# Performance work log

Hardware: AMD Instinct MI355X
Metric: run time of the kernel (lower is better)

## Reference

```python
import jax, jax.numpy as jnp
import numpy as np

IN_DIM = 1024
OUT_DIM = 1024
NUM_COEFFS = 32 + 3  # grid_size + spline_order


def setup_inputs() -> dict:
    key = jax.random.key(0)
    k1, k2, k3 = jax.random.split(key, 3)
    x = jax.random.normal(k1, (4096, IN_DIM), dtype=jnp.float32)
    spline_weight = jax.random.normal(k2, (IN_DIM, OUT_DIM, NUM_COEFFS), dtype=jnp.float32) * 0.1
    base_scale = jax.random.normal(k3, (IN_DIM, OUT_DIM), dtype=jnp.float32) * 0.1
    grid = jnp.linspace(-1.0, 1.0, NUM_COEFFS, dtype=jnp.float32)
    return {"x": x, "spline_weight": spline_weight, "base_scale": base_scale, "grid": grid}


def _b_spline_cubic(x, grid):
    # x: [b, i] -> basis [b, i, c]
    h = 2.0 / (NUM_COEFFS - 1)
    dist = jnp.abs(x[..., None] - grid) / h
    inner = 2.0 / 3.0 - dist * dist + dist * dist * dist * 0.5
    t = 2.0 - dist
    outer = t * t * t / 6.0
    return jnp.where(dist < 1.0, inner, jnp.where(dist < 2.0, outer, 0.0))


def reference(x, spline_weight, base_scale, grid):
    x_norm = jnp.clip(x, -0.99, 0.99)
    base_act = jax.nn.silu(x_norm)                      # [b, i]
    base_out = jnp.einsum('bi,ij->bj', base_act, base_scale)
    basis = _b_spline_cubic(x_norm, grid)               # [b, i, c]
    spline_out = jnp.einsum('bic,ijc->bj', basis, spline_weight)
    return base_out + spline_out
```

## Files before the change

### kernel.cpp

```cpp
#include <hip/hip_runtime.h>
#include <hip/hip_bf16.h>


#define IN_DIM 1024
#define OUT_DIM 1024
#define NC 35
#define KPI 36
#define KTOT (IN_DIM * KPI)
#define MROWS 4096
#define BM 128
#define BN 128
#define BK 32
#define BKP 40
#define NSPLIT 4
#define KCH (KTOT / NSPLIT)
#define NSTEP (KCH / BK)

typedef __attribute__((ext_vector_type(8))) __bf16 bf16x8;
typedef __attribute__((ext_vector_type(4))) float f32x4;

__device__ __forceinline__ unsigned short f2bf(float f) {
  unsigned int u = __builtin_bit_cast(unsigned int, f);
  u = (u + 0x7FFFu + ((u >> 16) & 1u)) >> 16;
  return (unsigned short)u;
}

__global__ __launch_bounds__(256) void prep_wb(const float* __restrict__ sw,
                                               const float* __restrict__ bs,
                                               unsigned short* __restrict__ wb) {
  int id = blockIdx.x * 256 + threadIdx.x;
  int i = id & (IN_DIM - 1);
  int n = id >> 10;
  const float* s = sw + (size_t)i * (OUT_DIM * NC) + (size_t)n * NC;
  unsigned short v[KPI];
#pragma unroll
  for (int c = 0; c < NC; ++c) v[c] = f2bf(s[c]);
  v[NC] = f2bf(bs[(size_t)i * OUT_DIM + n]);
  uint2* dst = (uint2*)(wb + (size_t)n * KTOT + (size_t)i * KPI);
#pragma unroll
  for (int w = 0; w < 9; ++w) {
    uint2 t;
    t.x = (unsigned)v[4 * w + 0] | ((unsigned)v[4 * w + 1] << 16);
    t.y = (unsigned)v[4 * w + 2] | ((unsigned)v[4 * w + 3] << 16);
    dst[w] = t;
  }
}

template <bool USE_WB>
__global__ __launch_bounds__(256) void kan_gemm(const float* __restrict__ x,
                                                const unsigned short* __restrict__ wb,
                                                const float* __restrict__ sw,
                                                const float* __restrict__ bs,
                                                float* __restrict__ out) {
  __shared__ __align__(16) unsigned short As[BM * BKP];
  __shared__ __align__(16) unsigned short Ws[BN * BKP];

  const int tid = threadIdx.x;
  const int mt = blockIdx.x, nt = blockIdx.y, kc = blockIdx.z;

  const int sb = tid & 127;
  const int shalf = tid >> 7;
  const int klo = shalf * 16;
  const int wrow = tid >> 1;
  const int whal = tid & 1;
  const int lane = tid & 63;
  const int wid = tid >> 6;
  const int wm = (wid & 1) * 64;
  const int wn = (wid >> 1) * 64;
  const int lm = lane & 15;
  const int quad = lane >> 4;
  const int ko = quad * 8;

  f32x4 acc[4][4];
#pragma unroll
  for (int a = 0; a < 4; ++a)
#pragma unroll
    for (int b = 0; b < 4; ++b) acc[a][b] = f32x4{0.f, 0.f, 0.f, 0.f};

  const float* xrow = x + (size_t)(mt * BM + sb) * IN_DIM;

  for (int step = 0; step < NSTEP; ++step) {
    const int kbase = kc * KCH + step * BK;

    {
      uint4 z = make_uint4(0, 0, 0, 0);
      uint4* az = (uint4*)(&As[sb * BKP + klo]);
      az[0] = z;
      az[1] = z;
    }

    {
      const int ilo = kbase / KPI;
      const int ihi = (kbase + BK - 1) / KPI;
      for (int ii = ilo; ii <= ihi; ++ii) {
        float xv = xrow[ii];
        float xn = fminf(fmaxf(xv, -0.99f), 0.99f);
        float u = (xn + 1.0f) * 17.0f;
        float sf = floorf(u);
        int s = (int)sf;
        float f = u - sf, g = 1.0f - f;
        float f2 = f * f, g2 = g * g;
        float v0 = g2 * g * (1.f / 6.f);
        float v1 = 0.66666667f - f2 + 0.5f * f2 * f;
        float v2 = 0.66666667f - g2 + 0.5f * g2 * g;
        float v3 = f2 * f * (1.f / 6.f);
        float sig = xn / (1.0f + __expf(-xn));
        const int kb0 = ii * KPI - kbase;
#pragma unroll
        for (int t = 0; t < 4; ++t) {
          int c = s - 1 + t;
          float v = (t == 0) ? v0 : (t == 1) ? v1 : (t == 2) ? v2 : v3;
          int kq = kb0 + c;
          if (c >= 0 && c < NC && kq >= klo && kq < klo + 16)
            As[sb * BKP + kq] = f2bf(v);
        }
        int kqb = kb0 + NC;
        if (kqb >= klo && kqb < klo + 16) As[sb * BKP + kqb] = f2bf(sig);
      }
    }

    if (USE_WB) {
      const unsigned short* src = wb + (size_t)(nt * BN + wrow) * KTOT + kbase + whal * 16;
      uint4 w0 = ((const uint4*)src)[0];
      uint4 w1 = ((const uint4*)src)[1];
      uint4* wd = (uint4*)(&Ws[wrow * BKP + whal * 16]);
      wd[0] = w0;
      wd[1] = w1;
    } else {
      const int j = nt * BN + wrow;
      unsigned int p[8];
#pragma unroll
      for (int q = 0; q < 8; ++q) {
        unsigned int lohi = 0;
#pragma unroll
        for (int h = 0; h < 2; ++h) {
          int k = kbase + whal * 16 + q * 2 + h;
          int i = k / KPI;
          int c = k - i * KPI;
          float v = (c < NC) ? sw[(size_t)i * (OUT_DIM * NC) + (size_t)j * NC + c]
                             : bs[(size_t)i * OUT_DIM + j];
          lohi |= ((unsigned int)f2bf(v)) << (16 * h);
        }
        p[q] = lohi;
      }
      uint4* wd = (uint4*)(&Ws[wrow * BKP + whal * 16]);
      wd[0] = make_uint4(p[0], p[1], p[2], p[3]);
      wd[1] = make_uint4(p[4], p[5], p[6], p[7]);
    }

    __syncthreads();

    uint4 af[4], bfr[4];
#pragma unroll
    for (int mi = 0; mi < 4; ++mi)
      af[mi] = *(const uint4*)(&As[(wm + mi * 16 + lm) * BKP + ko]);
#pragma unroll
    for (int ni = 0; ni < 4; ++ni)
      bfr[ni] = *(const uint4*)(&Ws[(wn + ni * 16 + lm) * BKP + ko]);
#pragma unroll
    for (int mi = 0; mi < 4; ++mi)
#pragma unroll
      for (int ni = 0; ni < 4; ++ni)
        acc[mi][ni] = __builtin_amdgcn_mfma_f32_16x16x32_bf16(
            __builtin_bit_cast(bf16x8, af[mi]), __builtin_bit_cast(bf16x8, bfr[ni]),
            acc[mi][ni], 0, 0, 0);

    __syncthreads();
  }

#pragma unroll
  for (int mi = 0; mi < 4; ++mi)
#pragma unroll
    for (int ni = 0; ni < 4; ++ni)
#pragma unroll
      for (int r = 0; r < 4; ++r) {
        int row = mt * BM + wm + mi * 16 + quad * 4 + r;
        int col = nt * BN + wn + ni * 16 + lm;
        atomicAdd(&out[(size_t)row * OUT_DIM + col], acc[mi][ni][r]);
      }
}

extern "C" void kernel_launch(void* const* d_in, const int* in_sizes, int n_in,
                              void* d_out, int out_size, void* d_ws, size_t ws_size,
                              hipStream_t stream) {
  const float* x = (const float*)d_in[0];
  const float* sw = (const float*)d_in[1];
  const float* bs = (const float*)d_in[2];
  float* out = (float*)d_out;

  hipMemsetAsync(d_out, 0, (size_t)MROWS * OUT_DIM * sizeof(float), stream);

  const size_t WB_BYTES = (size_t)OUT_DIM * KTOT * sizeof(unsigned short);
  dim3 grid(MROWS / BM, OUT_DIM / BN, NSPLIT);
  if (ws_size >= WB_BYTES) {
    unsigned short* wbp = (unsigned short*)d_ws;
    prep_wb<<<(IN_DIM * OUT_DIM) / 256, 256, 0, stream>>>(sw, bs, wbp);
    kan_gemm<true><<<grid, 256, 0, stream>>>(x, wbp, sw, bs, out);
  } else {
    kan_gemm<false><<<grid, 256, 0, stream>>>(x, nullptr, sw, bs, out);
  }
}
```

Measured before the change: 855.9 us.

## Materialize spline basis in workspace and pipeline GEMM with direct-to-LDS loads

Adds a prep kernel that expands x into the bf16 B-spline basis plus SiLU term. It writes the result to the workspace in a K-chunk-major layout, with weights repacked the same way. A new 256x256-tile GEMM with 512 threads then streams both operands through a triple-buffered LDS ring using global_load_lds, so loads overlap the MFMA work. This removes the redundant per-tile basis computation and the register round trips. In exchange it adds an extra ~300MB of workspace traffic and uses unpadded LDS rows, which may cause bank conflicts. It only takes effect if the workspace is large enough.

```diff
diff --git a/kernel.cpp b/kernel.cpp
--- a/kernel.cpp
+++ b/kernel.cpp
@@ -7,14 +7,13 @@
 #define NC 35
 #define KPI 36
 #define KTOT (IN_DIM * KPI)
+#define NW (KTOT / 32)
 #define MROWS 4096
-#define BM 128
-#define BN 128
+#define BM 256
+#define BN 256
 #define BK 32
-#define BKP 40
 #define NSPLIT 4
-#define KCH (KTOT / NSPLIT)
-#define NSTEP (KCH / BK)
+#define WPC (NW / NSPLIT)
 
 typedef __attribute__((ext_vector_type(8))) __bf16 bf16x8;
 typedef __attribute__((ext_vector_type(4))) float f32x4;
@@ -25,9 +24,199 @@
   return (unsigned short)u;
 }
 
-__global__ __launch_bounds__(256) void prep_wb(const float* __restrict__ sw,
-                                               const float* __restrict__ bs,
-                                               unsigned short* __restrict__ wb) {
+__global__ __launch_bounds__(256) void prep_w(const float* __restrict__ sw,
+                                              const float* __restrict__ bs,
+                                              unsigned short* __restrict__ w2) {
+  __shared__ float sbuf[2][256 * NC];
+  const int tid = threadIdx.x;
+  const int w = blockIdx.x;
+  const int n0 = blockIdx.y * 256;
+  const int k0 = w * 32;
+  const int i0 = k0 / KPI;
+  const int i1 = (k0 + 31) / KPI;
+  const int iq[2] = {i0, i1};
+  float bsv[2];
+#pragma unroll
+  for (int q = 0; q < 2; ++q) {
+    const float* src = sw + ((size_t)iq[q] * OUT_DIM + n0) * NC;
+    for (int t = tid; t < 256 * NC; t += 256) sbuf[q][t] = src[t];
+    bsv[q] = bs[(size_t)iq[q] * OUT_DIM + n0 + tid];
+  }
+  __syncthreads();
+  unsigned short v[32];
+#pragma unroll
+  for (int kk = 0; kk < 32; ++kk) {
+    int k = k0 + kk;
+    int q = (k >= (i0 + 1) * KPI) ? 1 : 0;
+    int c = k - iq[q] * KPI;
+    float f = (c < NC) ? sbuf[q][tid * NC + c] : bsv[q];
+    v[kk] = f2bf(f);
+  }
+  uint4* dst = (uint4*)(w2 + ((size_t)w * OUT_DIM + n0 + tid) * 32);
+#pragma unroll
+  for (int j = 0; j < 4; ++j) {
+    uint4 t4;
+    t4.x = (unsigned)v[8 * j + 0] | ((unsigned)v[8 * j + 1] << 16);
+    t4.y = (unsigned)v[8 * j + 2] | ((unsigned)v[8 * j + 3] << 16);
+    t4.z = (unsigned)v[8 * j + 4] | ((unsigned)v[8 * j + 5] << 16);
+    t4.w = (unsigned)v[8 * j + 6] | ((unsigned)v[8 * j + 7] << 16);
+    dst[j] = t4;
+  }
+}
+
+__global__ __launch_bounds__(256) void prep_a2(const float* __restrict__ x,
+                                               unsigned short* __restrict__ a2) {
+  const int tid = threadIdx.x;
+  const int w = blockIdx.x;
+  const int b = blockIdx.y * 256 + tid;
+  const int k0 = w * 32;
+  const int i0 = k0 / KPI;
+  const int i1 = (k0 + 31) / KPI;
+  const int iq[2] = {i0, i1};
+  int si[2];
+  float tv0[2], tv1[2], tv2[2], tv3[2], sg[2];
+#pragma unroll
+  for (int q = 0; q < 2; ++q) {
+    float xv = x[(size_t)b * IN_DIM + iq[q]];
+    float xn = fminf(fmaxf(xv, -0.99f), 0.99f);
+    float u = (xn + 1.0f) * 17.0f;
+    float sf = floorf(u);
+    si[q] = (int)sf;
+    float f = u - sf, g = 1.0f - f;
+    float f2 = f * f, g2 = g * g;
+    tv0[q] = g2 * g * (1.f / 6.f);
+    tv1[q] = 0.66666667f - f2 + 0.5f * f2 * f;
+    tv2[q] = 0.66666667f - g2 + 0.5f * g2 * g;
+    tv3[q] = f2 * f * (1.f / 6.f);
+    sg[q] = xn / (1.0f + __expf(-xn));
+  }
+  unsigned short v[32];
+#pragma unroll
+  for (int kk = 0; kk < 32; ++kk) {
+    int k = k0 + kk;
+    int q = (k >= (i0 + 1) * KPI) ? 1 : 0;
+    int c = k - iq[q] * KPI;
+    float val;
+    if (c == NC) {
+      val = sg[q];
+    } else {
+      int rel = c - (si[q] - 1);
+      val = (rel == 0) ? tv0[q]
+          : (rel == 1) ? tv1[q]
+          : (rel == 2) ? tv2[q]
+          : (rel == 3) ? tv3[q] : 0.0f;
+    }
+    v[kk] = f2bf(val);
+  }
+  uint4* dst = (uint4*)(a2 + ((size_t)w * MROWS + b) * 32);
+#pragma unroll
+  for (int j = 0; j < 4; ++j) {
+    uint4 t4;
+    t4.x = (unsigned)v[8 * j + 0] | ((unsigned)v[8 * j + 1] << 16);
+    t4.y = (unsigned)v[8 * j + 2] | ((unsigned)v[8 * j + 3] << 16);
+    t4.z = (unsigned)v[8 * j + 4] | ((unsigned)v[8 * j + 5] << 16);
+    t4.w = (unsigned)v[8 * j + 6] | ((unsigned)v[8 * j + 7] << 16);
+    dst[j] = t4;
+  }
+}
+
+__global__ __launch_bounds__(512) void kan_gemm3(const unsigned short* __restrict__ A2,
+                                                 const unsigned short* __restrict__ W2,
+                                                 float* __restrict__ out) {
+  __shared__ __align__(16) unsigned short As[3][BM * BK];
+  __shared__ __align__(16) unsigned short Ws[3][BN * BK];
+
+  const int tid = threadIdx.x;
+  const int mt = blockIdx.x, nt = blockIdx.y, kc = blockIdx.z;
+
+  const int lane = tid & 63;
+  const int wid = tid >> 6;
+  const int wm = (wid & 3) * 64;
+  const int wn = (wid >> 2) * 128;
+  const int lm = lane & 15;
+  const int quad = lane >> 4;
+  const int ko = quad * 8;
+
+  f32x4 acc[4][8];
+#pragma unroll
+  for (int a = 0; a < 4; ++a)
+#pragma unroll
+    for (int b = 0; b < 8; ++b) acc[a][b] = f32x4{0.f, 0.f, 0.f, 0.f};
+
+  const unsigned short* Abase = A2 + (size_t)(mt * BM) * 32 + lane * 8;
+  const unsigned short* Wbase = W2 + (size_t)(nt * BN) * 32 + lane * 8;
+
+  auto issue = [&](int buf, int w) {
+    const size_t aoff = (size_t)w * (MROWS * 32);
+    const size_t woff = (size_t)w * (OUT_DIM * 32);
+#pragma unroll
+    for (int c = 0; c < 2; ++c) {
+      const int g = wid * 2 + c;
+      __builtin_amdgcn_global_load_lds(
+          (const __attribute__((address_space(1))) unsigned int*)(Abase + aoff + (size_t)g * 512),
+          (__attribute__((address_space(3))) unsigned int*)(&As[buf][g * 512]),
+          16, 0, 0);
+      __builtin_amdgcn_global_load_lds(
+          (const __attribute__((address_space(1))) unsigned int*)(Wbase + woff + (size_t)g * 512),
+          (__attribute__((address_space(3))) unsigned int*)(&Ws[buf][g * 512]),
+          16, 0, 0);
+    }
+  };
+
+  issue(0, kc * WPC);
+  int cur = 0, nxt = 1;
+  for (int step = 0; step < WPC; ++step) {
+    if (step + 1 < WPC) {
+      issue(nxt, kc * WPC + step + 1);
+      asm volatile("s_waitcnt vmcnt(4) lgkmcnt(0)\ns_barrier" ::: "memory");
+    } else {
+      asm volatile("s_waitcnt vmcnt(0) lgkmcnt(0)\ns_barrier" ::: "memory");
+    }
+
+    uint4 af[4];
+#pragma unroll
+    for (int mi = 0; mi < 4; ++mi)
+      af[mi] = *(const uint4*)(&As[cur][(wm + mi * 16 + lm) * BK + ko]);
+#pragma unroll
+    for (int h = 0; h < 2; ++h) {
+      uint4 bfr[4];
+#pragma unroll
+      for (int nj = 0; nj < 4; ++nj)
+        bfr[nj] = *(const uint4*)(&Ws[cur][(wn + h * 64 + nj * 16 + lm) * BK + ko]);
+#pragma unroll
+      for (int mi = 0; mi < 4; ++mi)
+#pragma unroll
+        for (int nj = 0; nj < 4; ++nj)
+          acc[mi][h * 4 + nj] = __builtin_amdgcn_mfma_f32_16x16x32_bf16(
+              __builtin_bit_cast(bf16x8, af[mi]), __builtin_bit_cast(bf16x8, bfr[nj]),
+              acc[mi][h * 4 + nj], 0, 0, 0);
+    }
+
+    cur = nxt;
+    nxt = (nxt == 2) ? 0 : nxt + 1;
+  }
+
+#pragma unroll
+  for (int mi = 0; mi < 4; ++mi)
+#pragma unroll
+    for (int ni = 0; ni < 8; ++ni)
+#pragma unroll
+      for (int r = 0; r < 4; ++r) {
+        int row = mt * BM + wm + mi * 16 + quad * 4 + r;
+        int col = nt * BN + wn + ni * 16 + lm;
+        atomicAdd(&out[(size_t)row * OUT_DIM + col], acc[mi][ni][r]);
+      }
+}
+
+#define FB_BM 128
+#define FB_BN 128
+#define FB_BKPA 40
+#define FB_KCH 9216
+#define FB_NSTEP 288
+
+__global__ __launch_bounds__(256) void prep_wb_fb(const float* __restrict__ sw,
+                                                  const float* __restrict__ bs,
+                                                  unsigned short* __restrict__ wb) {
   int id = blockIdx.x * 256 + threadIdx.x;
   int i = id & (IN_DIM - 1);
   int n = id >> 10;
@@ -47,17 +236,16 @@
 }
 
 template <bool USE_WB>
-__global__ __launch_bounds__(256) void kan_gemm(const float* __restrict__ x,
-                                                const unsigned short* __restrict__ wb,
-                                                const float* __restrict__ sw,
-                                                const float* __restrict__ bs,
-                                                float* __restrict__ out) {
-  __shared__ __align__(16) unsigned short As[BM * BKP];
-  __shared__ __align__(16) unsigned short Ws[BN * BKP];
+__global__ __launch_bounds__(256) void kan_gemm_fb(const float* __restrict__ x,
+                                                   const unsigned short* __restrict__ wb,
+                                                   const float* __restrict__ sw,
+                                                   const float* __restrict__ bs,
+                                                   float* __restrict__ out) {
+  __shared__ __align__(16) unsigned short As[FB_BM * FB_BKPA];
+  __shared__ __align__(16) unsigned short Wsm[FB_BN * FB_BKPA];
 
   const int tid = threadIdx.x;
   const int mt = blockIdx.x, nt = blockIdx.y, kc = blockIdx.z;
-
   const int sb = tid & 127;
   const int shalf = tid >> 7;
   const int klo = shalf * 16;
@@ -77,18 +265,16 @@
 #pragma unroll
     for (int b = 0; b < 4; ++b) acc[a][b] = f32x4{0.f, 0.f, 0.f, 0.f};
 
-  const float* xrow = x + (size_t)(mt * BM + sb) * IN_DIM;
-
-  for (int step = 0; step < NSTEP; ++step) {
-    const int kbase = kc * KCH + step * BK;
-
+  const float* xrow = x + (size_t)(mt * FB_BM + sb) * IN_DIM;
+
+  for (int step = 0; step < FB_NSTEP; ++step) {
+    const int kbase = kc * FB_KCH + step * BK;
     {
       uint4 z = make_uint4(0, 0, 0, 0);
-      uint4* az = (uint4*)(&As[sb * BKP + klo]);
+      uint4* az = (uint4*)(&As[sb * FB_BKPA + klo]);
       az[0] = z;
       az[1] = z;
     }
-
     {
       const int ilo = kbase / KPI;
       const int ihi = (kbase + BK - 1) / KPI;
@@ -112,22 +298,21 @@
           float v = (t == 0) ? v0 : (t == 1) ? v1 : (t == 2) ? v2 : v3;
           int kq = kb0 + c;
           if (c >= 0 && c < NC && kq >= klo && kq < klo + 16)
-            As[sb * BKP + kq] = f2bf(v);
+            As[sb * FB_BKPA + kq] = f2bf(v);
         }
         int kqb = kb0 + NC;
-        if (kqb >= klo && kqb < klo + 16) As[sb * BKP + kqb] = f2bf(sig);
+        if (kqb >= klo && kqb < klo + 16) As[sb * FB_BKPA + kqb] = f2bf(sig);
       }
     }
-
     if (USE_WB) {
-      const unsigned short* src = wb + (size_t)(nt * BN + wrow) * KTOT + kbase + whal * 16;
+      const unsigned short* src = wb + (size_t)(nt * FB_BN + wrow) * KTOT + kbase + whal * 16;
       uint4 w0 = ((const uint4*)src)[0];
       uint4 w1 = ((const uint4*)src)[1];
-      uint4* wd = (uint4*)(&Ws[wrow * BKP + whal * 16]);
+      uint4* wd = (uint4*)(&Wsm[wrow * FB_BKPA + whal * 16]);
       wd[0] = w0;
       wd[1] = w1;
     } else {
-      const int j = nt * BN + wrow;
+      const int j = nt * FB_BN + wrow;
       unsigned int p[8];
 #pragma unroll
       for (int q = 0; q < 8; ++q) {
@@ -143,7 +328,7 @@
         }
         p[q] = lohi;
       }
-      uint4* wd = (uint4*)(&Ws[wrow * BKP + whal * 16]);
+      uint4* wd = (uint4*)(&Wsm[wrow * FB_BKPA + whal * 16]);
       wd[0] = make_uint4(p[0], p[1], p[2], p[3]);
       wd[1] = make_uint4(p[4], p[5], p[6], p[7]);
     }
@@ -153,10 +338,10 @@
     uint4 af[4], bfr[4];
 #pragma unroll
     for (int mi = 0; mi < 4; ++mi)
-      af[mi] = *(const uint4*)(&As[(wm + mi * 16 + lm) * BKP + ko]);
+      af[mi] = *(const uint4*)(&As[(wm + mi * 16 + lm) * FB_BKPA + ko]);
 #pragma unroll
     for (int ni = 0; ni < 4; ++ni)
-      bfr[ni] = *(const uint4*)(&Ws[(wn + ni * 16 + lm) * BKP + ko]);
+      bfr[ni] = *(const uint4*)(&Wsm[(wn + ni * 16 + lm) * FB_BKPA + ko]);
 #pragma unroll
     for (int mi = 0; mi < 4; ++mi)
 #pragma unroll
@@ -174,8 +359,8 @@
     for (int ni = 0; ni < 4; ++ni)
 #pragma unroll
       for (int r = 0; r < 4; ++r) {
-        int row = mt * BM + wm + mi * 16 + quad * 4 + r;
-        int col = nt * BN + wn + ni * 16 + lm;
+        int row = mt * FB_BM + wm + mi * 16 + quad * 4 + r;
+        int col = nt * FB_BN + wn + ni * 16 + lm;
         atomicAdd(&out[(size_t)row * OUT_DIM + col], acc[mi][ni][r]);
       }
 }
@@ -190,13 +375,20 @@
 
   hipMemsetAsync(d_out, 0, (size_t)MROWS * OUT_DIM * sizeof(float), stream);
 
-  const size_t WB_BYTES = (size_t)OUT_DIM * KTOT * sizeof(unsigned short);
-  dim3 grid(MROWS / BM, OUT_DIM / BN, NSPLIT);
-  if (ws_size >= WB_BYTES) {
+  const size_t WB_BYTES = (size_t)NW * OUT_DIM * 32 * sizeof(unsigned short);
+  const size_t A_BYTES = (size_t)NW * MROWS * 32 * sizeof(unsigned short);
+
+  if (ws_size >= WB_BYTES + A_BYTES) {
+    unsigned short* w2 = (unsigned short*)d_ws;
+    unsigned short* a2 = (unsigned short*)((char*)d_ws + WB_BYTES);
+    prep_w<<<dim3(NW, OUT_DIM / 256), 256, 0, stream>>>(sw, bs, w2);
+    prep_a2<<<dim3(NW, MROWS / 256), 256, 0, stream>>>(x, a2);
+    kan_gemm3<<<dim3(MROWS / BM, OUT_DIM / BN, NSPLIT), 512, 0, stream>>>(a2, w2, out);
+  } else if (ws_size >= WB_BYTES) {
     unsigned short* wbp = (unsigned short*)d_ws;
-    prep_wb<<<(IN_DIM * OUT_DIM) / 256, 256, 0, stream>>>(sw, bs, wbp);
-    kan_gemm<true><<<grid, 256, 0, stream>>>(x, wbp, sw, bs, out);
+    prep_wb_fb<<<(IN_DIM * OUT_DIM) / 256, 256, 0, stream>>>(sw, bs, wbp);
+    kan_gemm_fb<true><<<dim3(32, 8, 4), 256, 0, stream>>>(x, wbp, sw, bs, out);
   } else {
-    kan_gemm<false><<<grid, 256, 0, stream>>>(x, nullptr, sw, bs, out);
-  }
-}
+    kan_gemm_fb<false><<<dim3(32, 8, 4), 256, 0, stream>>>(x, nullptr, sw, bs, out);
+  }
+}
```

After: 717.7 us. 1.19x faster.
